# Kernel tuning notes

Measured on AMD Instinct MI355X. Metric: run time of the kernel, lower is better.

The kernel has to match this reference:

```python
import jax, jax.numpy as jnp
import numpy as np

B, S, IN_DIM, H_DIM, OUT_DIM, N_LAYERS = 64, 1024, 256, 512, 256, 2


def setup_inputs() -> dict:
    key = jax.random.key(0)
    ks = jax.random.split(key, 16)
    scale = 0.05

    def W(k, shape):
        return (jax.random.normal(k, shape, jnp.float32) * scale)

    inp = {
        "input": jax.random.normal(ks[0], (B, S, IN_DIM), jnp.float32),
        "hidden_state": jnp.zeros((B, N_LAYERS, H_DIM), jnp.float32),
    }
    ki = 1
    for i in range(N_LAYERS):
        d_in = IN_DIM if i == 0 else H_DIM
        for g in ("z", "r", "g"):
            inp[f"W{g}_in_{i}"] = W(ks[ki], (d_in, H_DIM)); ki += 1
            inp[f"W{g}_h_{i}"] = W(ks[ki], (H_DIM, H_DIM)); ki += 1
            inp[f"b{g}_{i}"] = jnp.zeros((H_DIM,), jnp.float32)
    inp["Wo"] = W(ks[ki], (H_DIM, OUT_DIM)); ki += 1
    inp["bo"] = jnp.zeros((OUT_DIM,), jnp.float32)
    return inp


def _gru_layer(xs, h0, Wzi, Wzh, bz, Wri, Wrh, br, Wgi, Wgh, bg):
    # Precompute input projections for all timesteps (same math as per-step Linear).
    xz = jnp.einsum("bsi,ih->bsh", xs, Wzi)
    xr = jnp.einsum("bsi,ih->bsh", xs, Wri)
    xg = jnp.einsum("bsi,ih->bsh", xs, Wgi)

    def step(h, t):
        xz_t, xr_t, xg_t = t
        z = jax.nn.sigmoid(xz_t + h @ Wzh + bz)
        r = jax.nn.sigmoid(xr_t + h @ Wrh + br)
        g = jnp.tanh(xg_t + (h * r) @ Wgh + bg)
        h_new = z * h + (1.0 - z) * g
        return h_new, h_new

    h_last, hs = jax.lax.scan(
        step, h0,
        (jnp.swapaxes(xz, 0, 1), jnp.swapaxes(xr, 0, 1), jnp.swapaxes(xg, 0, 1)))
    return jnp.swapaxes(hs, 0, 1), h_last  # (B,S,H), (B,H)


def reference(input, hidden_state,
              Wz_in_0, Wz_h_0, bz_0, Wr_in_0, Wr_h_0, br_0, Wg_in_0, Wg_h_0, bg_0,
              Wz_in_1, Wz_h_1, bz_1, Wr_in_1, Wr_h_1, br_1, Wg_in_1, Wg_h_1, bg_1,
              Wo, bo):
    layers = [
        (Wz_in_0, Wz_h_0, bz_0, Wr_in_0, Wr_h_0, br_0, Wg_in_0, Wg_h_0, bg_0),
        (Wz_in_1, Wz_h_1, bz_1, Wr_in_1, Wr_h_1, br_1, Wg_in_1, Wg_h_1, bg_1),
    ]
    b = input.shape[0]
    seq = input
    finals = []
    for i, p in enumerate(layers):
        seq, h_last = _gru_layer(seq, hidden_state[:, i, :], *p)
        finals.append(h_last)
    y = jnp.einsum("bsh,ho->bso", seq, Wo) + bo
    # Faithful to original: torch.cat(layer_states) then reshape to (B, L, H)
    h_out = jnp.concatenate(finals, axis=0).reshape(b, len(layers), H_DIM)
    return y, h_out
```

## Files before the change

kernel.cpp:

```cpp
#include <hip/hip_runtime.h>
#include <stdint.h>

typedef unsigned short u16;
typedef short v8s __attribute__((ext_vector_type(8)));
typedef float v4f __attribute__((ext_vector_type(4)));

#define B_ 64
#define S_ 1024
#define IN_ 256
#define H_ 512
#define OUT_ 256
#define BS_ (B_ * S_)
#define GS_ ((size_t)BS_ * H_)
#define HP_ (H_ + 8)
#define KP1_ (1024 + 8)
#define FPAD_ 16

static __device__ __forceinline__ u16 f2bf(float f) {
  uint32_t u = __float_as_uint(f);
  u += 0x7FFFu + ((u >> 16) & 1u);
  return (u16)(u >> 16);
}
static __device__ __forceinline__ float bf2f(u16 h) {
  return __uint_as_float(((uint32_t)h) << 16);
}
static __device__ __forceinline__ v4f mfma16(v8s a, v8s b, v4f c) {
  return __builtin_amdgcn_mfma_f32_16x16x32_bf16(a, b, c, 0, 0, 0);
}
static __device__ __forceinline__ uint64_t cload64(const uint64_t* p) {
  return __hip_atomic_load(p, __ATOMIC_RELAXED, __HIP_MEMORY_SCOPE_AGENT);
}
static __device__ __forceinline__ void cstore64(uint64_t* p, uint64_t v) {
  __hip_atomic_store(p, v, __ATOMIC_RELAXED, __HIP_MEMORY_SCOPE_AGENT);
}
static __device__ __forceinline__ void cstore32(uint32_t* p, uint32_t v) {
  __hip_atomic_store(p, v, __ATOMIC_RELAXED, __HIP_MEMORY_SCOPE_AGENT);
}
static __device__ __forceinline__ uint32_t cload32(const uint32_t* p) {
  return __hip_atomic_load(p, __ATOMIC_RELAXED, __HIP_MEMORY_SCOPE_AGENT);
}
template <int NS>
static __device__ __forceinline__ void slab_barrier(uint32_t* flagbase,
                                                    int slab, uint32_t want,
                                                    int tid) {
  __syncthreads();
  if (tid == 0)
    __hip_atomic_store(flagbase + slab * FPAD_, want, __ATOMIC_RELAXED,
                       __HIP_MEMORY_SCOPE_AGENT);
  if (tid < NS) {
    while (cload32(flagbase + tid * FPAD_) < want) __builtin_amdgcn_s_sleep(1);
  }
  __syncthreads();
}
static __device__ __forceinline__ void pack_store4(u16* dst, float v, int fr) {
  float o1 = __shfl_xor(v, 1);
  uint32_t c0 = f2bf(v), c1 = f2bf(o1);
  uint32_t pk = (fr & 1) ? (c1 | (c0 << 16)) : (c0 | (c1 << 16));
  uint32_t pk2 = __shfl_xor(pk, 2);
  if ((fr & 3) == 0)
    cstore64((uint64_t*)dst, (uint64_t)pk | ((uint64_t)pk2 << 32));
}

__global__ void cast_input_kernel(const float* __restrict__ src,
                                  u16* __restrict__ dst, int n4) {
  int i = blockIdx.x * blockDim.x + threadIdx.x;
  int stride = gridDim.x * blockDim.x;
  for (; i < n4; i += stride) {
    float4 v = ((const float4*)src)[i];
    uint32_t lo = (uint32_t)f2bf(v.x) | ((uint32_t)f2bf(v.y) << 16);
    uint32_t hi = (uint32_t)f2bf(v.z) | ((uint32_t)f2bf(v.w) << 16);
    ((uint2*)dst)[i] = make_uint2(lo, hi);
  }
}

__global__ void pack_transpose_k(const float* __restrict__ src,
                                 u16* __restrict__ dst, int K, int N,
                                 int dstK, int k0) {
  int i = blockIdx.x * blockDim.x + threadIdx.x;
  int total = K * N;
  int stride = gridDim.x * blockDim.x;
  for (; i < total; i += stride) {
    int n = i / K, k = i - n * K;
    dst[(size_t)n * dstK + k0 + k] = f2bf(src[(size_t)k * N + n]);
  }
}

__global__ void __launch_bounds__(256) gemm_kernel(
    const u16* __restrict__ A, const u16* __restrict__ Bt, int N, int K,
    u16* __restrict__ outb, float* __restrict__ outf,
    const float* __restrict__ bias, int mode) {
  const int bn = blockIdx.x * 64;
  const int bm = blockIdx.y * 64;
  const int w = threadIdx.x >> 6;
  const int lane = threadIdx.x & 63;
  const int wm = (w >> 1) * 32, wn = (w & 1) * 32;
  const int fr = lane & 15;
  const int kb = (lane >> 4) * 8;
  v4f acc00 = {0,0,0,0}, acc01 = {0,0,0,0}, acc10 = {0,0,0,0}, acc11 = {0,0,0,0};
  const u16* a0p = A + (size_t)(bm + wm + fr) * K + kb;
  const u16* a1p = a0p + (size_t)16 * K;
  const u16* b0p = Bt + (size_t)(bn + wn + fr) * K + kb;
  const u16* b1p = b0p + (size_t)16 * K;
  for (int kk = 0; kk < K; kk += 32) {
    v8s a0 = *(const v8s*)(a0p + kk);
    v8s a1 = *(const v8s*)(a1p + kk);
    v8s b0 = *(const v8s*)(b0p + kk);
    v8s b1 = *(const v8s*)(b1p + kk);
    acc00 = mfma16(a0, b0, acc00);
    acc01 = mfma16(a0, b1, acc01);
    acc10 = mfma16(a1, b0, acc10);
    acc11 = mfma16(a1, b1, acc11);
  }
  v4f accs[2][2] = {{acc00, acc01}, {acc10, acc11}};
  const int rb = (lane >> 4) * 4;
#pragma unroll
  for (int mi = 0; mi < 2; ++mi)
#pragma unroll
    for (int ni = 0; ni < 2; ++ni)
#pragma unroll
      for (int j = 0; j < 4; ++j) {
        int row = bm + wm + mi * 16 + rb + j;
        int col = bn + wn + ni * 16 + fr;
        float v = accs[mi][ni][j];
        if (mode == 0) {
          int gate = col >> 9, c = col & (H_ - 1);
          outb[(size_t)gate * GS_ + (size_t)row * H_ + c] = f2bf(v);
        } else {
          outf[(size_t)row * N + col] = v + bias[col];
        }
      }
}

__global__ void __launch_bounds__(256, 1) gru_pipe_kernel(
    const u16* xproj,
    const u16* __restrict__ Wht0,
    const u16* __restrict__ Wstk1,
    const float* __restrict__ bz0, const float* __restrict__ br0,
    const float* __restrict__ bg0,
    const float* __restrict__ bz1, const float* __restrict__ br1,
    const float* __restrict__ bg1,
    const float* __restrict__ hs,
    u16* h0buf,
    u16* hr0buf,
    u16* h1buf,
    u16* hr1buf,
    u16* seqout,
    float* __restrict__ hfinal,
    uint32_t* flags) {
  __shared__ __align__(16) char pool[134144];
  const int tid = threadIdx.x;
  const int bid = blockIdx.x;
  const int w = tid >> 6, lane = tid & 63;
  const int fr = lane & 15;
  const int kb = (lane >> 4) * 8;
  const int rb = (lane >> 4) * 4;

  if (bid < 64) {
    u16* ldsW = (u16*)pool;
    u16 (*ldsX)[HP_] = (u16(*)[HP_])(pool + 99840);
    float (*h32)[32] = (float(*)[32])(pool + 116480);
    const int grp = bid & 3;
    const int slab = bid >> 2;
    const int j0 = slab * 32;
    const int gb = grp * 16;

    for (int idx = tid; idx < 3 * 32 * 64; idx += 256) {
      int gate = idx >> 11;
      int rem = idx & 2047;
      int cl = rem >> 6;
      int kc = (rem & 63) * 8;
      *(v8s*)&ldsW[((gate * 32) + cl) * HP_ + kc] =
          *(const v8s*)(Wht0 + ((size_t)gate * H_ + (j0 + cl)) * H_ + kc);
    }
    for (int i = tid; i < 16 * H_; i += 256) {
      int row = i >> 9, col = i & (H_ - 1);
      ldsX[row][col] = f2bf(hs[((size_t)(gb + row) * 2 + 0) * H_ + col]);
    }
    for (int i = tid; i < 16 * 32; i += 256) {
      int row = i >> 5, cl = i & 31;
      h32[row][cl] = hs[((size_t)(gb + row) * 2 + 0) * H_ + j0 + cl];
    }
    __syncthreads();

    const int nt = w & 1;
    const int gateA = w >> 1;
    const int colL = nt * 16 + fr;
    const int gcol = j0 + colL;
    const float biasA = (gateA == 0) ? bz0[gcol] : br0[gcol];
    const float biasG = bg0[gcol];
    u16* hr0_g = hr0buf + (size_t)gb * H_;
    const u16* xA = xproj + (size_t)gateA * GS_;
    const u16* xG = xproj + (size_t)2 * GS_;
    const u16* wA = ldsW + ((size_t)(gateA * 32) + colL) * HP_;
    const u16* wG = ldsW + ((size_t)(2 * 32) + colL) * HP_;
    uint32_t* flagA0 = flags + (size_t)grp * 16 * FPAD_;
    uint32_t* flagB0 = flags + 1024 + (size_t)grp * 16 * FPAD_;
    uint32_t* c1gg   = flags + 6144 + (size_t)grp * 32 * FPAD_;

    float zv[4] = {0.f, 0.f, 0.f, 0.f};

    for (int t = 0; t < S_; ++t) {
      u16 xa_[4], xg_[4];
#pragma unroll
      for (int j = 0; j < 4; ++j) {
        size_t off = ((size_t)(gb + rb + j) * S_ + t) * H_ + gcol;
        xa_[j] = xA[off];
        if (w < 2) xg_[j] = xG[off];
      }

      if (t > 0) {
        if (w == 0) {
          const uint32_t* pa = flagB0;
          uint32_t want = 0;
          if (lane < 16) { pa = flagB0 + lane * FPAD_; want = (uint32_t)t; }
          else if (lane < 48) {
            pa = c1gg + (lane - 16) * FPAD_;
            if (t >= 4) want = (uint32_t)(t - 3);
          }
          while (cload32(pa) < want) __builtin_amdgcn_s_sleep(1);
        }
        __syncthreads();
        const uint64_t* src =
            (const uint64_t*)(h0buf + ((size_t)((t - 1) & 3) * B_ + gb) * H_);
        uint64_t vq[8];
#pragma unroll
        for (int i = 0; i < 8; ++i) vq[i] = cload64(src + i * 256 + tid);
#pragma unroll
        for (int i = 0; i < 8; ++i) {
          int d = i * 256 + tid;
          *(uint64_t*)&ldsX[d >> 7][(d & 127) * 4] = vq[i];
        }
        __syncthreads();
      }

      v4f acc0 = {0,0,0,0}, acc1 = {0,0,0,0};
#pragma unroll
      for (int kk = 0; kk < 8; ++kk) {
        acc0 = mfma16(*(const v8s*)&ldsX[fr][kk * 32 + kb],
                      *(const v8s*)(wA + kk * 32 + kb), acc0);
        acc1 = mfma16(*(const v8s*)&ldsX[fr][256 + kk * 32 + kb],
                      *(const v8s*)(wA + 256 + kk * 32 + kb), acc1);
      }
      float pre[4];
#pragma unroll
      for (int j = 0; j < 4; ++j) {
        float s = acc0[j] + acc1[j] + bf2f(xa_[j]) + biasA;
        pre[j] = 1.0f / (1.0f + __expf(-s));
      }
      if (gateA == 0) {
#pragma unroll
        for (int j = 0; j < 4; ++j) zv[j] = pre[j];
      } else {
#pragma unroll
        for (int j = 0; j < 4; ++j)
          pack_store4(&hr0_g[(size_t)(rb + j) * H_ + gcol],
                      pre[j] * h32[rb + j][colL], fr);
      }
      asm volatile("s_waitcnt vmcnt(0)" ::: "memory");
      slab_barrier<16>(flagA0, slab, (uint32_t)(t + 1), tid);

      {
        const uint64_t* src = (const uint64_t*)hr0_g;
        uint64_t vq[8];
#pragma unroll
        for (int i = 0; i < 8; ++i) vq[i] = cload64(src + i * 256 + tid);
#pragma unroll
        for (int i = 0; i < 8; ++i) {
          int d = i * 256 + tid;
          *(uint64_t*)&ldsX[d >> 7][(d & 127) * 4] = vq[i];
        }
        __syncthreads();
      }

      if (w < 2) {
        v4f g0 = {0,0,0,0}, g1 = {0,0,0,0};
#pragma unroll
        for (int kk = 0; kk < 8; ++kk) {
          g0 = mfma16(*(const v8s*)&ldsX[fr][kk * 32 + kb],
                      *(const v8s*)(wG + kk * 32 + kb), g0);
          g1 = mfma16(*(const v8s*)&ldsX[fr][256 + kk * 32 + kb],
                      *(const v8s*)(wG + 256 + kk * 32 + kb), g1);
        }
        u16* h0dst = h0buf + ((size_t)(t & 3) * B_ + gb) * H_;
#pragma unroll
        for (int j = 0; j < 4; ++j) {
          int b = gb + rb + j;
          float gval = tanhf(g0[j] + g1[j] + bf2f(xg_[j]) + biasG);
          float hold = h32[rb + j][colL];
          float hnew = zv[j] * hold + (1.0f - zv[j]) * gval;
          h32[rb + j][colL] = hnew;
          pack_store4(&h0dst[(size_t)(rb + j) * H_ + gcol], hnew, fr);
          if (t == S_ - 1) hfinal[(size_t)b * H_ + gcol] = hnew;
        }
      }
      asm volatile("s_waitcnt vmcnt(0)" ::: "memory");
      __syncthreads();
      if (tid == 0)
        cstore32(flagB0 + slab * FPAD_, (uint32_t)(t + 1));
    }
  } else {
    u16* ldsW = (u16*)pool;
    u16 (*ldsX)[KP1_] = (u16(*)[KP1_])(pool + 99072);
    float (*h32b)[16] = (float(*)[16])(pool + 132096);
    float (*xg32)[16] = (float(*)[16])(pool + 133120);
    const int b2 = bid - 64;
    const int grp = b2 & 3;
    const int slab = b2 >> 2;
    const int j0 = slab * 16;
    const int gb = grp * 16;
    const int gcol = j0 + fr;

    for (int idx = tid; idx < 3 * 16 * 128; idx += 256) {
      int gate = idx >> 11;
      int rem = idx & 2047;
      int cl = rem >> 7;
      int kc = (rem & 127) * 8;
      *(v8s*)&ldsW[((gate * 16) + cl) * KP1_ + kc] =
          *(const v8s*)(Wstk1 + ((size_t)(gate * H_) + (j0 + cl)) * 1024 + kc);
    }
    for (int i = tid; i < 16 * H_; i += 256) {
      int row = i >> 9, col = i & (H_ - 1);
      ldsX[row][512 + col] = f2bf(hs[((size_t)(gb + row) * 2 + 1) * H_ + col]);
    }
    for (int i = tid; i < 16 * 16; i += 256) {
      int row = i >> 4, c = i & 15;
      h32b[row][c] = hs[((size_t)(gb + row) * 2 + 1) * H_ + j0 + c];
    }
    __syncthreads();

    const float bzv = bz1[gcol], brv = br1[gcol], bgv = bg1[gcol];
    u16* h1_g = h1buf + (size_t)gb * H_;
    u16* hr1_g = hr1buf + (size_t)gb * H_;
    const u16* wZ = ldsW + ((size_t)(0 * 16) + fr) * KP1_;
    const u16* wR = ldsW + ((size_t)(1 * 16) + fr) * KP1_;
    const u16* wG = ldsW + ((size_t)(2 * 16) + fr) * KP1_;
    uint32_t* flagB0 = flags + 1024 + (size_t)grp * 16 * FPAD_;
    uint32_t* flagA1 = flags + 2048 + (size_t)grp * 32 * FPAD_;
    uint32_t* flagB1 = flags + 4096 + (size_t)grp * 32 * FPAD_;
    uint32_t* c1gg   = flags + 6144 + (size_t)grp * 32 * FPAD_;
    float* hf1 = hfinal + (size_t)B_ * H_;

    float zv[4] = {0.f, 0.f, 0.f, 0.f};

    for (int t = 0; t < S_; ++t) {
      if (w == 0) {
        const uint32_t* pa = flagB0;
        uint32_t want = 0;
        if (lane < 16) { pa = flagB0 + lane * FPAD_; want = (uint32_t)(t + 1); }
        else if (lane < 48) {
          pa = flagB1 + (lane - 16) * FPAD_;
          want = (uint32_t)t;
        }
        while (cload32(pa) < want) __builtin_amdgcn_s_sleep(1);
      }
      __syncthreads();
      {
        const uint64_t* s0 =
            (const uint64_t*)(h0buf + ((size_t)((t & 3)) * B_ + gb) * H_);
        uint64_t q0[8];
#pragma unroll
        for (int i = 0; i < 8; ++i) q0[i] = cload64(s0 + i * 256 + tid);
        if (t > 0) {
          const uint64_t* s1 = (const uint64_t*)h1_g;
          uint64_t q1[8];
#pragma unroll
          for (int i = 0; i < 8; ++i) q1[i] = cload64(s1 + i * 256 + tid);
#pragma unroll
          for (int i = 0; i < 8; ++i) {
            int d = i * 256 + tid;
            *(uint64_t*)&ldsX[d >> 7][512 + (d & 127) * 4] = q1[i];
          }
        }
#pragma unroll
        for (int i = 0; i < 8; ++i) {
          int d = i * 256 + tid;
          *(uint64_t*)&ldsX[d >> 7][(d & 127) * 4] = q0[i];
        }
      }
      __syncthreads();
      if (tid == 0) cstore32(&c1gg[slab * FPAD_], (uint32_t)(t + 1));

      if (w < 2) {
        const u16* wB = (w == 0) ? wZ : wR;
        v4f a0 = {0,0,0,0}, a1 = {0,0,0,0}, a2 = {0,0,0,0}, a3 = {0,0,0,0};
#pragma unroll
        for (int kk = 0; kk < 8; ++kk) {
          a0 = mfma16(*(const v8s*)&ldsX[fr][kk * 32 + kb],
                      *(const v8s*)(wB + kk * 32 + kb), a0);
          a1 = mfma16(*(const v8s*)&ldsX[fr][256 + kk * 32 + kb],
                      *(const v8s*)(wB + 256 + kk * 32 + kb), a1);
          a2 = mfma16(*(const v8s*)&ldsX[fr][512 + kk * 32 + kb],
                      *(const v8s*)(wB + 512 + kk * 32 + kb), a2);
          a3 = mfma16(*(const v8s*)&ldsX[fr][768 + kk * 32 + kb],
                      *(const v8s*)(wB + 768 + kk * 32 + kb), a3);
        }
        float pre[4];
#pragma unroll
        for (int j = 0; j < 4; ++j) {
          float s = a0[j] + a1[j] + a2[j] + a3[j] + ((w == 0) ? bzv : brv);
          pre[j] = 1.0f / (1.0f + __expf(-s));
        }
        if (w == 0) {
#pragma unroll
          for (int j = 0; j < 4; ++j) zv[j] = pre[j];
        } else {
#pragma unroll
          for (int j = 0; j < 4; ++j)
            pack_store4(&hr1_g[(size_t)(rb + j) * H_ + gcol],
                        pre[j] * h32b[rb + j][fr], fr);
        }
      } else if (w == 2) {
        v4f a0 = {0,0,0,0}, a1 = {0,0,0,0};
#pragma unroll
        for (int kk = 0; kk < 8; ++kk) {
          a0 = mfma16(*(const v8s*)&ldsX[fr][kk * 32 + kb],
                      *(const v8s*)(wG + kk * 32 + kb), a0);
          a1 = mfma16(*(const v8s*)&ldsX[fr][256 + kk * 32 + kb],
                      *(const v8s*)(wG + 256 + kk * 32 + kb), a1);
        }
#pragma unroll
        for (int j = 0; j < 4; ++j) xg32[rb + j][fr] = a0[j] + a1[j];
      }
      asm volatile("s_waitcnt vmcnt(0)" ::: "memory");
      slab_barrier<32>(flagA1, slab, (uint32_t)(t + 1), tid);

      {
        const uint64_t* sr = (const uint64_t*)hr1_g;
        uint64_t q[8];
#pragma unroll
        for (int i = 0; i < 8; ++i) q[i] = cload64(sr + i * 256 + tid);
#pragma unroll
        for (int i = 0; i < 8; ++i) {
          int d = i * 256 + tid;
          *(uint64_t*)&ldsX[d >> 7][512 + (d & 127) * 4] = q[i];
        }
        __syncthreads();
      }

      uint64_t qsv[4];
      float hn[4];
      if (w == 0) {
        v4f g0 = {0,0,0,0}, g1 = {0,0,0,0};
#pragma unroll
        for (int kk = 0; kk < 8; ++kk) {
          g0 = mfma16(*(const v8s*)&ldsX[fr][512 + kk * 32 + kb],
                      *(const v8s*)(wG + 512 + kk * 32 + kb), g0);
          g1 = mfma16(*(const v8s*)&ldsX[fr][768 + kk * 32 + kb],
                      *(const v8s*)(wG + 768 + kk * 32 + kb), g1);
        }
#pragma unroll
        for (int j = 0; j < 4; ++j) {
          float gval = tanhf(g0[j] + g1[j] + xg32[rb + j][fr] + bgv);
          float hold = h32b[rb + j][fr];
          float hnew = zv[j] * hold + (1.0f - zv[j]) * gval;
          h32b[rb + j][fr] = hnew;
          hn[j] = hnew;
          float o1 = __shfl_xor(hnew, 1);
          uint32_t c0 = f2bf(hnew), c1 = f2bf(o1);
          uint32_t pk = (fr & 1) ? (c1 | (c0 << 16)) : (c0 | (c1 << 16));
          uint32_t pk2 = __shfl_xor(pk, 2);
          uint64_t qv = (uint64_t)pk | ((uint64_t)pk2 << 32);
          qsv[j] = qv;
          if ((fr & 3) == 0)
            cstore64((uint64_t*)&h1_g[(size_t)(rb + j) * H_ + gcol], qv);
        }
      }
      asm volatile("s_waitcnt vmcnt(0)" ::: "memory");
      __syncthreads();
      if (tid == 0) cstore32(flagB1 + slab * FPAD_, (uint32_t)(t + 1));

      if (w == 0) {
#pragma unroll
        for (int j = 0; j < 4; ++j) {
          int b = gb + rb + j;
          if ((fr & 3) == 0)
            *(uint64_t*)&seqout[((size_t)b * S_ + t) * H_ + gcol] = qsv[j];
          if (t == S_ - 1) hf1[(size_t)b * H_ + gcol] = hn[j];
        }
      }
    }
  }
}

extern "C" void kernel_launch(void* const* d_in, const int* in_sizes, int n_in,
                              void* d_out, int out_size, void* d_ws,
                              size_t ws_size, hipStream_t stream) {
  const float* input = (const float*)d_in[0];
  const float* hs = (const float*)d_in[1];
  const float* W_in[2][3] = {
      {(const float*)d_in[2], (const float*)d_in[5], (const float*)d_in[8]},
      {(const float*)d_in[11], (const float*)d_in[14], (const float*)d_in[17]}};
  const float* W_h[2][3] = {
      {(const float*)d_in[3], (const float*)d_in[6], (const float*)d_in[9]},
      {(const float*)d_in[12], (const float*)d_in[15], (const float*)d_in[18]}};
  const float* bias[2][3] = {
      {(const float*)d_in[4], (const float*)d_in[7], (const float*)d_in[10]},
      {(const float*)d_in[13], (const float*)d_in[16], (const float*)d_in[19]}};
  const float* Wo = (const float*)d_in[20];
  const float* bo = (const float*)d_in[21];
  float* out = (float*)d_out;

  char* ws = (char*)d_ws;
  u16* xproj   = (u16*)(ws + 0);
  u16* wtin0   = (u16*)(ws + 201326592);
  u16* wth0    = (u16*)(ws + 202113024);
  u16* wstk1   = (u16*)(ws + 203685888);
  u16* wot     = (u16*)(ws + 206831616);
  u16* h0buf   = (u16*)(ws + 207093760);
  u16* hr0buf  = (u16*)(ws + 207355904);
  u16* h1buf   = (u16*)(ws + 207421440);
  u16* hr1buf  = (u16*)(ws + 207486976);
  uint32_t* flags = (uint32_t*)(ws + 207552512);

  u16* inbf = (u16*)d_out;
  u16* seq2 = xproj;

  cast_input_kernel<<<2048, 256, 0, stream>>>(input, inbf, BS_ * IN_ / 4);

  for (int g = 0; g < 3; ++g) {
    pack_transpose_k<<<256, 256, 0, stream>>>(
        W_in[0][g], wtin0 + (size_t)g * H_ * IN_, IN_, H_, IN_, 0);
    pack_transpose_k<<<256, 256, 0, stream>>>(
        W_h[0][g], wth0 + (size_t)g * H_ * H_, H_, H_, H_, 0);
    pack_transpose_k<<<256, 256, 0, stream>>>(
        W_in[1][g], wstk1 + (size_t)g * H_ * 1024, H_, H_, 1024, 0);
    pack_transpose_k<<<256, 256, 0, stream>>>(
        W_h[1][g], wstk1 + (size_t)g * H_ * 1024, H_, H_, 1024, 512);
  }
  pack_transpose_k<<<256, 256, 0, stream>>>(Wo, wot, H_, OUT_, H_, 0);

  gemm_kernel<<<dim3(24, 1024), 256, 0, stream>>>(
      inbf, wtin0, 1536, IN_, xproj, nullptr, nullptr, 0);

  hipMemsetAsync(flags, 0, 32768, stream);
  const size_t ysz = (size_t)BS_ * OUT_;
  float* hfin = out + ysz;
  gru_pipe_kernel<<<dim3(192), dim3(256), 0, stream>>>(
      xproj, wth0, wstk1, bias[0][0], bias[0][1], bias[0][2], bias[1][0],
      bias[1][1], bias[1][2], hs, h0buf, hr0buf, h1buf, hr1buf, seq2, hfin,
      flags);

  gemm_kernel<<<dim3(4, 1024), 256, 0, stream>>>(seq2, wot, OUT_, H_, nullptr,
                                                 out, bo, 1);
}
```

Before: 6.686 ms.

## Load MFMA hidden-state fragments directly from global memory, drop LDS staging

Rather than cooperatively copying the shared hidden-state and h*r buffers into LDS and syncing before each matmul, each wave now loads its MFMA A-fragments straight from global memory into registers with relaxed atomic loads. This removes several __syncthreads and LDS round trips per timestep, plus the layer-1 c1gg flag, which the layer-0 wait now replaces by polling flagA1. The cost is redundant global/L2 reads across waves (each wave loads the full 16x512 tile), higher register pressure from 16-32 v8s fragments, and the t==0 case converting fp32 initial state inline.

```diff
diff --git a/kernel.cpp b/kernel.cpp
--- a/kernel.cpp
+++ b/kernel.cpp
@@ -38,6 +38,19 @@
 }
 static __device__ __forceinline__ uint32_t cload32(const uint32_t* p) {
   return __hip_atomic_load(p, __ATOMIC_RELAXED, __HIP_MEMORY_SCOPE_AGENT);
+}
+static __device__ __forceinline__ v8s frag_ex(const u16* rowbase, int off) {
+  union { uint64_t q[2]; v8s v; } u;
+  const uint64_t* p = (const uint64_t*)(rowbase + off);
+  u.q[0] = cload64(p);
+  u.q[1] = cload64(p + 1);
+  return u.v;
+}
+static __device__ __forceinline__ v8s frag_f32(const float* rowbase, int off) {
+  union { u16 h[8]; v8s v; } u;
+#pragma unroll
+  for (int e = 0; e < 8; ++e) u.h[e] = f2bf(rowbase[off + e]);
+  return u.v;
 }
 template <int NS>
 static __device__ __forceinline__ void slab_barrier(uint32_t* flagbase,
@@ -147,7 +160,7 @@
     u16* seqout,
     float* __restrict__ hfinal,
     uint32_t* flags) {
-  __shared__ __align__(16) char pool[134144];
+  __shared__ __align__(16) char pool[101888];
   const int tid = threadIdx.x;
   const int bid = blockIdx.x;
   const int w = tid >> 6, lane = tid & 63;
@@ -157,8 +170,7 @@
 
   if (bid < 64) {
     u16* ldsW = (u16*)pool;
-    u16 (*ldsX)[HP_] = (u16(*)[HP_])(pool + 99840);
-    float (*h32)[32] = (float(*)[32])(pool + 116480);
+    float (*h32)[32] = (float(*)[32])(pool + 99840);
     const int grp = bid & 3;
     const int slab = bid >> 2;
     const int j0 = slab * 32;
@@ -171,10 +183,6 @@
       int kc = (rem & 63) * 8;
       *(v8s*)&ldsW[((gate * 32) + cl) * HP_ + kc] =
           *(const v8s*)(Wht0 + ((size_t)gate * H_ + (j0 + cl)) * H_ + kc);
-    }
-    for (int i = tid; i < 16 * H_; i += 256) {
-      int row = i >> 9, col = i & (H_ - 1);
-      ldsX[row][col] = f2bf(hs[((size_t)(gb + row) * 2 + 0) * H_ + col]);
     }
     for (int i = tid; i < 16 * 32; i += 256) {
       int row = i >> 5, cl = i & 31;
@@ -195,7 +203,8 @@
     const u16* wG = ldsW + ((size_t)(2 * 32) + colL) * HP_;
     uint32_t* flagA0 = flags + (size_t)grp * 16 * FPAD_;
     uint32_t* flagB0 = flags + 1024 + (size_t)grp * 16 * FPAD_;
-    uint32_t* c1gg   = flags + 6144 + (size_t)grp * 32 * FPAD_;
+    uint32_t* flagA1 = flags + 2048 + (size_t)grp * 32 * FPAD_;
+    const float* hrow0f = &hs[((size_t)(gb + fr) * 2 + 0) * H_];
 
     float zv[4] = {0.f, 0.f, 0.f, 0.f};
 
@@ -214,32 +223,30 @@
           uint32_t want = 0;
           if (lane < 16) { pa = flagB0 + lane * FPAD_; want = (uint32_t)t; }
           else if (lane < 48) {
-            pa = c1gg + (lane - 16) * FPAD_;
+            pa = flagA1 + (lane - 16) * FPAD_;
             if (t >= 4) want = (uint32_t)(t - 3);
           }
           while (cload32(pa) < want) __builtin_amdgcn_s_sleep(1);
         }
         __syncthreads();
-        const uint64_t* src =
-            (const uint64_t*)(h0buf + ((size_t)((t - 1) & 3) * B_ + gb) * H_);
-        uint64_t vq[8];
-#pragma unroll
-        for (int i = 0; i < 8; ++i) vq[i] = cload64(src + i * 256 + tid);
-#pragma unroll
-        for (int i = 0; i < 8; ++i) {
-          int d = i * 256 + tid;
-          *(uint64_t*)&ldsX[d >> 7][(d & 127) * 4] = vq[i];
-        }
-        __syncthreads();
-      }
-
+      }
+
+      v8s hf[16];
+      if (t == 0) {
+#pragma unroll
+        for (int kk = 0; kk < 16; ++kk)
+          hf[kk] = frag_f32(hrow0f, kk * 32 + kb);
+      } else {
+        const u16* hsrc =
+            h0buf + (((size_t)((t - 1) & 3)) * B_ + gb + fr) * H_;
+#pragma unroll
+        for (int kk = 0; kk < 16; ++kk) hf[kk] = frag_ex(hsrc, kk * 32 + kb);
+      }
       v4f acc0 = {0,0,0,0}, acc1 = {0,0,0,0};
 #pragma unroll
       for (int kk = 0; kk < 8; ++kk) {
-        acc0 = mfma16(*(const v8s*)&ldsX[fr][kk * 32 + kb],
-                      *(const v8s*)(wA + kk * 32 + kb), acc0);
-        acc1 = mfma16(*(const v8s*)&ldsX[fr][256 + kk * 32 + kb],
-                      *(const v8s*)(wA + 256 + kk * 32 + kb), acc1);
+        acc0 = mfma16(hf[kk], *(const v8s*)(wA + kk * 32 + kb), acc0);
+        acc1 = mfma16(hf[8 + kk], *(const v8s*)(wA + 256 + kk * 32 + kb), acc1);
       }
       float pre[4];
 #pragma unroll
@@ -259,27 +266,16 @@
       asm volatile("s_waitcnt vmcnt(0)" ::: "memory");
       slab_barrier<16>(flagA0, slab, (uint32_t)(t + 1), tid);
 
-      {
-        const uint64_t* src = (const uint64_t*)hr0_g;
-        uint64_t vq[8];
-#pragma unroll
-        for (int i = 0; i < 8; ++i) vq[i] = cload64(src + i * 256 + tid);
-#pragma unroll
-        for (int i = 0; i < 8; ++i) {
-          int d = i * 256 + tid;
-          *(uint64_t*)&ldsX[d >> 7][(d & 127) * 4] = vq[i];
-        }
-        __syncthreads();
-      }
-
       if (w < 2) {
+        const u16* hrsrc = hr0_g + (size_t)fr * H_;
+        v8s rf[16];
+#pragma unroll
+        for (int kk = 0; kk < 16; ++kk) rf[kk] = frag_ex(hrsrc, kk * 32 + kb);
         v4f g0 = {0,0,0,0}, g1 = {0,0,0,0};
 #pragma unroll
         for (int kk = 0; kk < 8; ++kk) {
-          g0 = mfma16(*(const v8s*)&ldsX[fr][kk * 32 + kb],
-                      *(const v8s*)(wG + kk * 32 + kb), g0);
-          g1 = mfma16(*(const v8s*)&ldsX[fr][256 + kk * 32 + kb],
-                      *(const v8s*)(wG + 256 + kk * 32 + kb), g1);
+          g0 = mfma16(rf[kk], *(const v8s*)(wG + kk * 32 + kb), g0);
+          g1 = mfma16(rf[8 + kk], *(const v8s*)(wG + 256 + kk * 32 + kb), g1);
         }
         u16* h0dst = h0buf + ((size_t)(t & 3) * B_ + gb) * H_;
 #pragma unroll
@@ -295,14 +291,12 @@
       }
       asm volatile("s_waitcnt vmcnt(0)" ::: "memory");
       __syncthreads();
-      if (tid == 0)
-        cstore32(flagB0 + slab * FPAD_, (uint32_t)(t + 1));
+      if (tid == 0) cstore32(flagB0 + slab * FPAD_, (uint32_t)(t + 1));
     }
   } else {
     u16* ldsW = (u16*)pool;
-    u16 (*ldsX)[KP1_] = (u16(*)[KP1_])(pool + 99072);
-    float (*h32b)[16] = (float(*)[16])(pool + 132096);
-    float (*xg32)[16] = (float(*)[16])(pool + 133120);
+    float (*h32b)[16] = (float(*)[16])(pool + 99072);
+    float (*xg32)[16] = (float(*)[16])(pool + 100096);
     const int b2 = bid - 64;
     const int grp = b2 & 3;
     const int slab = b2 >> 2;
@@ -317,10 +311,6 @@
       int kc = (rem & 127) * 8;
       *(v8s*)&ldsW[((gate * 16) + cl) * KP1_ + kc] =
           *(const v8s*)(Wstk1 + ((size_t)(gate * H_) + (j0 + cl)) * 1024 + kc);
-    }
-    for (int i = tid; i < 16 * H_; i += 256) {
-      int row = i >> 9, col = i & (H_ - 1);
-      ldsX[row][512 + col] = f2bf(hs[((size_t)(gb + row) * 2 + 1) * H_ + col]);
     }
     for (int i = tid; i < 16 * 16; i += 256) {
       int row = i >> 4, c = i & 15;
@@ -337,8 +327,8 @@
     uint32_t* flagB0 = flags + 1024 + (size_t)grp * 16 * FPAD_;
     uint32_t* flagA1 = flags + 2048 + (size_t)grp * 32 * FPAD_;
     uint32_t* flagB1 = flags + 4096 + (size_t)grp * 32 * FPAD_;
-    uint32_t* c1gg   = flags + 6144 + (size_t)grp * 32 * FPAD_;
-    float* hf1 = hfinal + (size_t)B_ * H_;
+    float* hf1out = hfinal + (size_t)B_ * H_;
+    const float* hrow1f = &hs[((size_t)(gb + fr) * 2 + 1) * H_];
 
     float zv[4] = {0.f, 0.f, 0.f, 0.f};
 
@@ -354,45 +344,30 @@
         while (cload32(pa) < want) __builtin_amdgcn_s_sleep(1);
       }
       __syncthreads();
-      {
-        const uint64_t* s0 =
-            (const uint64_t*)(h0buf + ((size_t)((t & 3)) * B_ + gb) * H_);
-        uint64_t q0[8];
-#pragma unroll
-        for (int i = 0; i < 8; ++i) q0[i] = cload64(s0 + i * 256 + tid);
-        if (t > 0) {
-          const uint64_t* s1 = (const uint64_t*)h1_g;
-          uint64_t q1[8];
-#pragma unroll
-          for (int i = 0; i < 8; ++i) q1[i] = cload64(s1 + i * 256 + tid);
-#pragma unroll
-          for (int i = 0; i < 8; ++i) {
-            int d = i * 256 + tid;
-            *(uint64_t*)&ldsX[d >> 7][512 + (d & 127) * 4] = q1[i];
-          }
-        }
-#pragma unroll
-        for (int i = 0; i < 8; ++i) {
-          int d = i * 256 + tid;
-          *(uint64_t*)&ldsX[d >> 7][(d & 127) * 4] = q0[i];
-        }
-      }
-      __syncthreads();
-      if (tid == 0) cstore32(&c1gg[slab * FPAD_], (uint32_t)(t + 1));
+
+      const u16* s0 = h0buf + (((size_t)(t & 3)) * B_ + gb + fr) * H_;
 
       if (w < 2) {
+        v8s f0[16], f1[16];
+#pragma unroll
+        for (int kk = 0; kk < 16; ++kk) f0[kk] = frag_ex(s0, kk * 32 + kb);
+        if (t == 0) {
+#pragma unroll
+          for (int kk = 0; kk < 16; ++kk)
+            f1[kk] = frag_f32(hrow1f, kk * 32 + kb);
+        } else {
+          const u16* s1 = h1_g + (size_t)fr * H_;
+#pragma unroll
+          for (int kk = 0; kk < 16; ++kk) f1[kk] = frag_ex(s1, kk * 32 + kb);
+        }
         const u16* wB = (w == 0) ? wZ : wR;
         v4f a0 = {0,0,0,0}, a1 = {0,0,0,0}, a2 = {0,0,0,0}, a3 = {0,0,0,0};
 #pragma unroll
         for (int kk = 0; kk < 8; ++kk) {
-          a0 = mfma16(*(const v8s*)&ldsX[fr][kk * 32 + kb],
-                      *(const v8s*)(wB + kk * 32 + kb), a0);
-          a1 = mfma16(*(const v8s*)&ldsX[fr][256 + kk * 32 + kb],
-                      *(const v8s*)(wB + 256 + kk * 32 + kb), a1);
-          a2 = mfma16(*(const v8s*)&ldsX[fr][512 + kk * 32 + kb],
-                      *(const v8s*)(wB + 512 + kk * 32 + kb), a2);
-          a3 = mfma16(*(const v8s*)&ldsX[fr][768 + kk * 32 + kb],
-                      *(const v8s*)(wB + 768 + kk * 32 + kb), a3);
+          a0 = mfma16(f0[kk], *(const v8s*)(wB + kk * 32 + kb), a0);
+          a1 = mfma16(f0[8 + kk], *(const v8s*)(wB + 256 + kk * 32 + kb), a1);
+          a2 = mfma16(f1[kk], *(const v8s*)(wB + 512 + kk * 32 + kb), a2);
+          a3 = mfma16(f1[8 + kk], *(const v8s*)(wB + 768 + kk * 32 + kb), a3);
         }
         float pre[4];
 #pragma unroll
@@ -410,43 +385,33 @@
                         pre[j] * h32b[rb + j][fr], fr);
         }
       } else if (w == 2) {
+        v8s f0[16];
+#pragma unroll
+        for (int kk = 0; kk < 16; ++kk) f0[kk] = frag_ex(s0, kk * 32 + kb);
         v4f a0 = {0,0,0,0}, a1 = {0,0,0,0};
 #pragma unroll
         for (int kk = 0; kk < 8; ++kk) {
-          a0 = mfma16(*(const v8s*)&ldsX[fr][kk * 32 + kb],
-                      *(const v8s*)(wG + kk * 32 + kb), a0);
-          a1 = mfma16(*(const v8s*)&ldsX[fr][256 + kk * 32 + kb],
-                      *(const v8s*)(wG + 256 + kk * 32 + kb), a1);
+          a0 = mfma16(f0[kk], *(const v8s*)(wG + kk * 32 + kb), a0);
+          a1 = mfma16(f0[8 + kk], *(const v8s*)(wG + 256 + kk * 32 + kb), a1);
         }
 #pragma unroll
         for (int j = 0; j < 4; ++j) xg32[rb + j][fr] = a0[j] + a1[j];
       }
       asm volatile("s_waitcnt vmcnt(0)" ::: "memory");
       slab_barrier<32>(flagA1, slab, (uint32_t)(t + 1), tid);
-
-      {
-        const uint64_t* sr = (const uint64_t*)hr1_g;
-        uint64_t q[8];
-#pragma unroll
-        for (int i = 0; i < 8; ++i) q[i] = cload64(sr + i * 256 + tid);
-#pragma unroll
-        for (int i = 0; i < 8; ++i) {
-          int d = i * 256 + tid;
-          *(uint64_t*)&ldsX[d >> 7][512 + (d & 127) * 4] = q[i];
-        }
-        __syncthreads();
-      }
 
       uint64_t qsv[4];
       float hn[4];
       if (w == 0) {
+        const u16* hrsrc = hr1_g + (size_t)fr * H_;
+        v8s rf[16];
+#pragma unroll
+        for (int kk = 0; kk < 16; ++kk) rf[kk] = frag_ex(hrsrc, kk * 32 + kb);
         v4f g0 = {0,0,0,0}, g1 = {0,0,0,0};
 #pragma unroll
         for (int kk = 0; kk < 8; ++kk) {
-          g0 = mfma16(*(const v8s*)&ldsX[fr][512 + kk * 32 + kb],
-                      *(const v8s*)(wG + 512 + kk * 32 + kb), g0);
-          g1 = mfma16(*(const v8s*)&ldsX[fr][768 + kk * 32 + kb],
-                      *(const v8s*)(wG + 768 + kk * 32 + kb), g1);
+          g0 = mfma16(rf[kk], *(const v8s*)(wG + 512 + kk * 32 + kb), g0);
+          g1 = mfma16(rf[8 + kk], *(const v8s*)(wG + 768 + kk * 32 + kb), g1);
         }
 #pragma unroll
         for (int j = 0; j < 4; ++j) {
@@ -475,7 +440,7 @@
           int b = gb + rb + j;
           if ((fr & 3) == 0)
             *(uint64_t*)&seqout[((size_t)b * S_ + t) * H_ + gcol] = qsv[j];
-          if (t == S_ - 1) hf1[(size_t)b * H_ + gcol] = hn[j];
+          if (t == S_ - 1) hf1out[(size_t)b * H_ + gcol] = hn[j];
         }
       }
     }
```

New measurement: 10.67 ms. 1.6x slower.
